# Kernel tuning notes

Measured on AMD Instinct MI355X. Metric: run time of the kernel, lower is better.

Reference implementation:

```python
import jax, jax.numpy as jnp
import numpy as np

T, B = 512, 256
OBS, FEAT, H, ACT = 128, 512, 256, 16
LOG2PI = float(np.log(2.0 * np.pi))


def layer_norm(x, w, b, eps=1e-5):
    m = x.mean(-1, keepdims=True)
    v = ((x - m) ** 2).mean(-1, keepdims=True)
    return (x - m) / jnp.sqrt(v + eps) * w + b


def mlp_features(x, W1, b1, W2, b2, gw, gb):
    h = jax.nn.relu(x @ W1.T + b1)
    h = layer_norm(h @ W2.T + b2, gw, gb)
    return jax.nn.relu(h)


def masked_lstm_scan(feat, done, h0, c0, Wih, Whh, bih, bhh):
    # feat: [T,B,H], done: [T,B] float, h0/c0: [B,H]. PyTorch gate order i,f,g,o.
    def step(carry, inp):
        h, c = carry
        x, d = inp
        m = (1.0 - d)[:, None]
        h = h * m
        c = c * m
        g = x @ Wih.T + bih + h @ Whh.T + bhh
        i, f, gg, o = jnp.split(g, 4, axis=-1)
        c = jax.nn.sigmoid(f) * c + jax.nn.sigmoid(i) * jnp.tanh(gg)
        h = jax.nn.sigmoid(o) * jnp.tanh(c)
        return (h, c), h
    (hT, cT), hs = jax.lax.scan(step, (h0, c0), (feat, done))
    return hs, hT, cT


def setup_inputs():
    key = jax.random.key(0)
    ks = jax.random.split(key, 40)
    rn = lambda k, s, sc=0.05: jax.random.normal(k, s, dtype=jnp.float32) * sc
    inp = {}
    inp["x"] = jax.random.normal(ks[0], (T * B, OBS), dtype=jnp.float32)
    inp["done"] = jax.random.randint(ks[1], (T * B,), 0, 2).astype(jnp.int32)
    inp["actor_h0"] = rn(ks[2], (1, B, H), 0.1)
    inp["actor_c0"] = rn(ks[3], (1, B, H), 0.1)
    inp["critic_h0"] = rn(ks[4], (1, B, H), 0.1)
    inp["critic_c0"] = rn(ks[5], (1, B, H), 0.1)
    inp["action"] = jax.random.normal(ks[6], (T * B, ACT), dtype=jnp.float32)
    j = 7
    for p in ("a", "c"):
        inp[p + "_W1"] = rn(ks[j], (FEAT, OBS)); j += 1
        inp[p + "_b1"] = jnp.zeros((FEAT,), jnp.float32)
        inp[p + "_W2"] = rn(ks[j], (H, FEAT)); j += 1
        inp[p + "_b2"] = jnp.zeros((H,), jnp.float32)
        inp[p + "_flnw"] = jnp.ones((H,), jnp.float32)
        inp[p + "_flnb"] = jnp.zeros((H,), jnp.float32)
        inp[p + "_Wih"] = rn(ks[j], (4 * H, H)); j += 1
        inp[p + "_Whh"] = rn(ks[j], (4 * H, H)); j += 1
        inp[p + "_bih"] = jnp.zeros((4 * H,), jnp.float32)
        inp[p + "_bhh"] = jnp.zeros((4 * H,), jnp.float32)
        inp[p + "_lnw"] = jnp.ones((H,), jnp.float32)
        inp[p + "_lnb"] = jnp.zeros((H,), jnp.float32)
    inp["a_mW"] = rn(ks[j], (ACT, H)); j += 1
    inp["a_mb"] = jnp.zeros((ACT,), jnp.float32)
    inp["a_logstd"] = jnp.zeros((1, ACT), jnp.float32)
    inp["c_hW"] = rn(ks[j], (1, H)); j += 1
    inp["c_hb"] = jnp.zeros((1,), jnp.float32)
    return inp


def reference(x, done, actor_h0, actor_c0, critic_h0, critic_c0, action,
              a_W1, a_b1, a_W2, a_b2, a_flnw, a_flnb, a_Wih, a_Whh, a_bih, a_bhh,
              a_lnw, a_lnb, a_mW, a_mb, a_logstd,
              c_W1, c_b1, c_W2, c_b2, c_flnw, c_flnb, c_Wih, c_Whh, c_bih, c_bhh,
              c_lnw, c_lnb, c_hW, c_hb):
    Bn = actor_h0.shape[1]
    N = x.shape[0]
    Tn = N // Bn
    d = done.astype(jnp.float32).reshape(Tn, Bn)
    # actor branch
    a_feat = mlp_features(x, a_W1, a_b1, a_W2, a_b2, a_flnw, a_flnb).reshape(Tn, Bn, -1)
    hs, ah, acell = masked_lstm_scan(a_feat, d, actor_h0[0], actor_c0[0], a_Wih, a_Whh, a_bih, a_bhh)
    ha = layer_norm(hs.reshape(N, -1), a_lnw, a_lnb)
    mean = ha @ a_mW.T + a_mb
    logstd = jnp.broadcast_to(a_logstd, mean.shape)
    std = jnp.exp(logstd)
    logprob = (-0.5 * ((action - mean) / std) ** 2 - logstd - 0.5 * LOG2PI).sum(1)
    entropy = (0.5 + 0.5 * LOG2PI + logstd).sum(1)
    # critic branch
    c_feat = mlp_features(x, c_W1, c_b1, c_W2, c_b2, c_flnw, c_flnb).reshape(Tn, Bn, -1)
    cs, ch, ccell = masked_lstm_scan(c_feat, d, critic_h0[0], critic_c0[0], c_Wih, c_Whh, c_bih, c_bhh)
    hc = layer_norm(cs.reshape(N, -1), c_lnw, c_lnb)
    value = hc @ c_hW.T + c_hb
    return (logprob, entropy, value, ah[None], acell[None], ch[None], ccell[None])
```

## Files before the change

### kernel.cpp

```cpp
#include <hip/hip_runtime.h>

typedef unsigned short u16;
typedef unsigned long long u64;
typedef __attribute__((ext_vector_type(8))) short short8;
typedef __attribute__((ext_vector_type(4))) float floatx4;
typedef __attribute__((ext_vector_type(4))) float f32x4;
typedef __attribute__((ext_vector_type(4))) int intx4;

#define LOG2PI_F 1.8378770664093453f
#define LOG2E_F 1.4426950408889634f
#define TWOLOG2E_F 2.8853900817779268f

__device__ inline float bf2f(u16 u) { return __uint_as_float(((unsigned)u) << 16); }
__device__ inline u16 f2bf(float f) {
  unsigned u = __float_as_uint(f);
  u += 0x7fff + ((u >> 16) & 1);
  return (u16)(u >> 16);
}

struct PrepArgs {
  const float* src[18];
  const float* src2[18];
  void* dst[18];
  int mode[18];
  int n[18];
  int blk0[19];
  int nseg;
};

__global__ __launch_bounds__(256) void k_prep(PrepArgs a) {
  int b = blockIdx.x, s = 0;
  while (s + 1 < a.nseg && b >= a.blk0[s + 1]) ++s;
  int i = (b - a.blk0[s]) * 1024 + threadIdx.x * 4;
  if (i >= a.n[s]) return;
  if (a.mode[s] == 0) {
    f32x4 v = *(const f32x4*)(a.src[s] + i);
    u64 p = (u64)f2bf(v[0]) | ((u64)f2bf(v[1]) << 16)
          | ((u64)f2bf(v[2]) << 32) | ((u64)f2bf(v[3]) << 48);
    *(u64*)((u16*)a.dst[s] + i) = p;
  } else if (a.mode[s] == 1) {
    f32x4 x = *(const f32x4*)(a.src[s] + i);
    f32x4 y = *(const f32x4*)(a.src2[s] + i);
    *(f32x4*)((float*)a.dst[s] + i) = x + y;
  } else {
    *(f32x4*)((float*)a.dst[s] + i) = *(const f32x4*)(a.src[s] + i);
  }
}

__global__ __launch_bounds__(256) void k_quant(const float* __restrict__ w0,
                                               const float* __restrict__ w1,
                                               char* __restrict__ q, float* __restrict__ sr) {
  int tid = threadIdx.x, lane = tid & 63;
  int row = blockIdx.x * 4 + (tid >> 6);
  int br = row >> 10, r = row & 1023;
  const float* src = (br ? w1 : w0) + (size_t)r * 256 + lane * 4;
  f32x4 v = *(const f32x4*)src;
  float m = fmaxf(fmaxf(fabsf(v[0]), fabsf(v[1])), fmaxf(fabsf(v[2]), fabsf(v[3])));
#pragma unroll
  for (int o = 32; o >= 1; o >>= 1) m = fmaxf(m, __shfl_xor(m, o));
  float inv = m > 0.f ? 127.f / m : 0.f;
  int pk = 0;
#pragma unroll
  for (int c = 0; c < 4; ++c) {
    int qq = __float2int_rn(v[c] * inv);
    qq = qq > 127 ? 127 : (qq < -127 ? -127 : qq);
    pk |= (qq & 255) << (8 * c);
  }
  *(int*)(q + (size_t)row * 256 + lane * 4) = pk;
  if (lane == 0) {
    float sf = (r >= 512 && r < 768) ? TWOLOG2E_F : -LOG2E_F;
    sr[row] = m * (1.f / (127.f * 127.f)) * sf;
  }
}

template <int EPI, int AF32>
__global__ __launch_bounds__(256, 2) void k_gemm(
    const void* __restrict__ Agv, const u16* __restrict__ Wg,
    const float* __restrict__ biasP, void* __restrict__ outv,
    int Nn, int K, int relu, int Tseg,
    long az, long wz, long oz) {
  __shared__ u16 As[128][72];
  __shared__ u16 Ws[128][72];
  const int tid = threadIdx.x;
  const int z = blockIdx.z;
  const int bn = blockIdx.x * 128;
  const int bm = blockIdx.y * 128;
  const int w = tid >> 6, lane = tid & 63, lm = lane & 15, lq = lane >> 4;
  const int wr = (w >> 1) * 64, wc = (w & 1) * 64;
  const int tr = tid >> 3, tc = (tid & 7) * 8;

  const u16* Ab = (const u16*)Agv;
  const float* Af = (const float*)Agv;
  const u16* Wb = Wg + (size_t)z * wz;

  floatx4 acc[4][4] = {};

  for (int k0 = 0; k0 < K; k0 += 64) {
    __syncthreads();
#pragma unroll
    for (int rr = 0; rr < 4; ++rr) {
      int row = rr * 32 + tr;
      if (AF32) {
        const float* src = Af + (size_t)z * az + (size_t)(bm + row) * K + k0 + tc;
        f32x4 v0 = *(const f32x4*)src;
        f32x4 v1 = *(const f32x4*)(src + 4);
        short8 sv;
#pragma unroll
        for (int c = 0; c < 4; ++c) { sv[c] = (short)f2bf(v0[c]); sv[4 + c] = (short)f2bf(v1[c]); }
        *(short8*)&As[row][tc] = sv;
      } else {
        *(short8*)&As[row][tc] = *(const short8*)(Ab + (size_t)z * az + (size_t)(bm + row) * K + k0 + tc);
      }
      *(short8*)&Ws[row][tc] = *(const short8*)(Wb + (size_t)(bn + row) * K + k0 + tc);
    }
    __syncthreads();
#pragma unroll
    for (int kk = 0; kk < 2; ++kk) {
      short8 a4[4], b4[4];
#pragma unroll
      for (int i = 0; i < 4; ++i) {
        a4[i] = *(const short8*)&As[wr + i * 16 + lm][kk * 32 + lq * 8];
        b4[i] = *(const short8*)&Ws[wc + i * 16 + lm][kk * 32 + lq * 8];
      }
#pragma unroll
      for (int i = 0; i < 4; ++i)
#pragma unroll
        for (int j = 0; j < 4; ++j)
          acc[i][j] = __builtin_amdgcn_mfma_f32_16x16x32_bf16(a4[i], b4[j], acc[i][j], 0, 0, 0);
    }
  }

#pragma unroll
  for (int i = 0; i < 4; ++i) {
#pragma unroll
    for (int j = 0; j < 4; ++j) {
      int col = bn + wc + j * 16 + lm;
      float bv = biasP[(size_t)z * Nn + col];
      float v[4];
#pragma unroll
      for (int r = 0; r < 4; ++r) {
        float t = acc[i][j][r] + bv;
        v[r] = relu ? fmaxf(t, 0.f) : t;
      }
      int row0l = bm + wr + i * 16 + lq * 4;
      if (EPI == 1) {
        u16* o = (u16*)outv + (size_t)z * oz;
#pragma unroll
        for (int r = 0; r < 4; ++r) o[(size_t)(row0l + r) * Nn + col] = f2bf(v[r]);
      } else {
        float s = (col >= 512 && col < 768) ? TWOLOG2E_F : -LOG2E_F;
        int t_l = row0l >> 8;
        int bfull = row0l & 255;
        int bbx = bfull >> 4;
        int mq = (bfull >> 2) & 3;
        u64 p = (u64)f2bf(v[0] * s) | ((u64)f2bf(v[1] * s) << 16)
              | ((u64)f2bf(v[2] * s) << 32) | ((u64)f2bf(v[3] * s) << 48);
        u16* o = (u16*)outv + (size_t)z * oz;
        size_t idx = ((((size_t)bbx * Tseg + t_l) * 4 + mq) * 1024 + col) * 4;
        *(u64*)(o + idx) = p;
      }
    }
  }
}

__global__ __launch_bounds__(256) void k_ln_relu(const u16* __restrict__ in,
                                                 const float* __restrict__ lnp,
                                                 u16* __restrict__ out,
                                                 long inz, long outz) {
  int z = blockIdx.y;
  int w = threadIdx.x >> 6, lane = threadIdx.x & 63;
  size_t row = (size_t)blockIdx.x * 4 + w;
  const u16* ip = in + (size_t)z * inz;
  u16* op = out + (size_t)z * outz;
  const float* gw = lnp + (size_t)z * 512;
  const float* gb = gw + 256;
  u64 hv = *(const u64*)(ip + row * 256 + lane * 4);
  float x[4];
#pragma unroll
  for (int c = 0; c < 4; ++c) x[c] = bf2f((u16)(hv >> (16 * c)));
  float s = x[0] + x[1] + x[2] + x[3];
  float q = x[0] * x[0] + x[1] * x[1] + x[2] * x[2] + x[3] * x[3];
#pragma unroll
  for (int o = 32; o >= 1; o >>= 1) { s += __shfl_xor(s, o); q += __shfl_xor(q, o); }
  float mean = s * (1.f / 256.f);
  float var = q * (1.f / 256.f) - mean * mean;
  float rs = rsqrtf(var + 1e-5f);
  u64 p = 0;
#pragma unroll
  for (int c = 0; c < 4; ++c) {
    int k = lane * 4 + c;
    float y = (x[c] - mean) * rs * gw[k] + gb[k];
    y = fmaxf(y, 0.f);
    p |= ((u64)f2bf(y)) << (16 * c);
  }
  *(u64*)(op + row * 256 + lane * 4) = p;
}

struct ScanArgs {
  const u16 *gin0, *gin1;
  const char *whq0, *whq1;
  const float *sr0, *sr1;
  const float *h00, *h01, *c00, *c01;
  char *hs0, *hs1;
  float *hsv0, *hsv1, *csv0, *csv1;
  const int* done;
  int t0, Tseg;
};

__global__ __launch_bounds__(1024, 1) void k_scan(ScanArgs A) {
  const int bb = blockIdx.x & 127, br = blockIdx.x >> 7;
  const int bbx = bb >> 3;
  const int rb = bb << 1;
  const int tid = threadIdx.x;
  const int w = tid >> 6, lane = tid & 63, lm = lane & 15, lq = lane >> 4;
  const int mrow = lq & 1;
  const bool iscell = lq < 2;
  const int jj = w * 16 + lm;
  const int hoff = w * 256 + mrow * 16 + lm;

  extern __shared__ char dsm[];
  char* hl = dsm;

  const char* whq = br ? A.whq1 : A.whq0;
  const float* srP = br ? A.sr1 : A.sr0;
  const u16* gin = (br ? A.gin1 : A.gin0) + (size_t)bbx * A.Tseg * 16384;
  const float* h0 = br ? A.h01 : A.h00;
  const float* c0 = br ? A.c01 : A.c00;
  char* hs = (br ? A.hs1 : A.hs0) + bbx * 4096;
  float* hsv = br ? A.hsv1 : A.hsv0;
  float* csv = br ? A.csv1 : A.csv0;

  intx4 wreg[4][4];
#pragma unroll
  for (int g = 0; g < 4; ++g)
#pragma unroll
    for (int kk = 0; kk < 4; ++kk)
      wreg[g][kk] =
          *(const intx4*)(whq + (size_t)(g * 256 + w * 16 + lm) * 256 + kk * 64 + lq * 16);

  float srw[4];
#pragma unroll
  for (int g = 0; g < 4; ++g) srw[g] = srP[g * 256 + jj];

  float creg = c0[(size_t)(rb + mrow) * 256 + jj];

  if (tid < 512) {
    int c = tid & 255, buf = tid >> 8;
    int kk = c >> 6, lqk = (c >> 4) & 3, m = c & 15;
    intx4 val = {0, 0, 0, 0};
    if (buf == 0 && m < 2) {
      const float* hp = h0 + (size_t)(rb + m) * 256 + kk * 64 + lqk * 16;
#pragma unroll
      for (int q4 = 0; q4 < 4; ++q4) {
        int pk = 0;
#pragma unroll
        for (int b = 0; b < 4; ++b) {
          int qv = __float2int_rn(hp[q4 * 4 + b] * 127.f);
          qv = qv > 127 ? 127 : (qv < -127 ? -127 : qv);
          pk |= (qv & 255) << (8 * b);
        }
        val[q4] = pk;
      }
    }
    *(intx4*)&hl[buf * 4096 + c * 16] = val;
  }
  __syncthreads();

  const u16* ginT = gin + ((rb >> 2) & 3) * 4096 + (rb & 3) + mrow + jj * 4;
  const int* dptrA = A.done + (size_t)A.t0 * 256 + rb + (lm & 1);
  const int* dptrC = A.done + (size_t)A.t0 * 256 + rb + mrow;

  u16 gnxt[4] = {0, 0, 0, 0};
  int dcN = 0;
  int daN = *dptrA;
  if (iscell) {
#pragma unroll
    for (int g = 0; g < 4; ++g) gnxt[g] = ginT[g * 1024];
    dcN = *dptrC;
  }

  intx4 z4 = {0, 0, 0, 0};

  for (int tl = 0; tl < A.Tseg; ++tl) {
    const int curo = (tl & 1) * 4096, nxto = curo ^ 4096;

    u16 gcur[4];
#pragma unroll
    for (int g = 0; g < 4; ++g) gcur[g] = gnxt[g];
    int da = daN;
    int dc = dcN;

    if (tl + 1 < A.Tseg) {
      ginT += 16384;
      dptrA += 256;
      dptrC += 256;
      daN = *dptrA;
      if (iscell) {
#pragma unroll
        for (int g = 0; g < 4; ++g) gnxt[g] = ginT[g * 1024];
        dcN = *dptrC;
      }
    }

    intx4 af[4];
#pragma unroll
    for (int kk = 0; kk < 4; ++kk) {
      intx4 hv = *(const intx4*)&hl[curo + kk * 1024 + lane * 16];
      af[kk] = da ? z4 : hv;
    }

    intx4 acc[4] = {};
#pragma unroll
    for (int kk = 0; kk < 4; ++kk)
#pragma unroll
      for (int g = 0; g < 4; ++g)
        acc[g] = __builtin_amdgcn_mfma_i32_16x16x64_i8(af[kk], wreg[g][kk], acc[g], 0, 0, 0);

    int av[4];
#pragma unroll
    for (int g = 0; g < 4; ++g) {
      int s0 = __shfl(acc[g][0], lm);
      int s1 = __shfl(acc[g][1], lm);
      av[g] = mrow ? s1 : s0;
    }

    if (iscell) {
      float cprev = dc ? 0.f : creg;
      float xi = fmaf((float)av[0], srw[0], bf2f(gcur[0]));
      float xf = fmaf((float)av[1], srw[1], bf2f(gcur[1]));
      float xg = fmaf((float)av[2], srw[2], bf2f(gcur[2]));
      float xo = fmaf((float)av[3], srw[3], bf2f(gcur[3]));
      float ig = __builtin_amdgcn_rcpf(1.f + __builtin_amdgcn_exp2f(xi));
      float fg = __builtin_amdgcn_rcpf(1.f + __builtin_amdgcn_exp2f(xf));
      float gg = 1.f - 2.f * __builtin_amdgcn_rcpf(1.f + __builtin_amdgcn_exp2f(xg));
      float og = __builtin_amdgcn_rcpf(1.f + __builtin_amdgcn_exp2f(xo));
      float cn = fg * cprev + ig * gg;
      creg = cn;
      float th = 1.f - 2.f * __builtin_amdgcn_rcpf(1.f + __builtin_amdgcn_exp2f(TWOLOG2E_F * cn));
      float hn = og * th;
      int qv = __float2int_rn(hn * 127.f);
      hl[nxto + hoff] = (char)qv;
      if (tl == A.Tseg - 1) {
        size_t idx = (size_t)(rb + mrow) * 256 + jj;
        hsv[idx] = hn;
        csv[idx] = cn;
      }
    }
    asm volatile("s_waitcnt lgkmcnt(0)" ::: "memory");
    __builtin_amdgcn_s_barrier();
    __builtin_amdgcn_sched_barrier(0);
    if (tid < 128) {
      int a_l = nxto + (tid >> 3) * 256 + (tid & 7) * 4;
      int mg = (bb & 7) * 2 + ((tid >> 2) & 1);
      int a_g = (tid >> 3) * 256 + mg * 16 + (tid & 3) * 4;
      *(int*)(hs + (size_t)tl * 65536 + a_g) = *(const int*)&hl[a_l];
    }
  }
}

__global__ __launch_bounds__(256) void k_head(
    const char* __restrict__ hs_a, const char* __restrict__ hs_c,
    const float* __restrict__ a_lnw, const float* __restrict__ a_lnb,
    const float* __restrict__ c_lnw, const float* __restrict__ c_lnb,
    const float* __restrict__ mW, const float* __restrict__ mb,
    const float* __restrict__ logstd, const float* __restrict__ hW,
    const float* __restrict__ hb, const float* __restrict__ action,
    float* __restrict__ lp, float* __restrict__ ent, float* __restrict__ val,
    int row0) {
  __shared__ float smW[16][260];
  __shared__ float shW[256];
  __shared__ float spar[4][256];
  __shared__ float hrow[4][264];
  int tid = threadIdx.x;
  for (int i = tid; i < 4096; i += 256) smW[i >> 8][i & 255] = mW[i];
  shW[tid] = hW[tid];
  spar[0][tid] = a_lnw[tid]; spar[1][tid] = a_lnb[tid];
  spar[2][tid] = c_lnw[tid]; spar[3][tid] = c_lnb[tid];
  __syncthreads();

  int w = tid >> 6, lane = tid & 63, lm = lane & 15, lq = lane >> 4;
  float entc = 0.f;
#pragma unroll
  for (int j = 0; j < 16; ++j) entc += 0.5f + 0.5f * LOG2PI_F + logstd[j];
  float ls = logstd[lm];
  float sd = __expf(ls);
  float mbj = mb[lm];

  int rbase = (blockIdx.x * 4 + w) * 16;
  for (int rr = 0; rr < 16; ++rr) {
    int row = rbase + rr;
    int m = row & 15;
    size_t base = (size_t)(row >> 8) * 65536 + (size_t)((row >> 4) & 15) * 4096;
    int off = (lane >> 4) * 1024 + (m + 16 * ((lane >> 2) & 3)) * 16 + (lane & 3) * 4;
    int va = *(const int*)(hs_a + base + off);
    float x[4];
#pragma unroll
    for (int c = 0; c < 4; ++c) x[c] = (float)((va << (24 - 8 * c)) >> 24) * (1.f / 127.f);
    float s = x[0] + x[1] + x[2] + x[3];
    float q = x[0] * x[0] + x[1] * x[1] + x[2] * x[2] + x[3] * x[3];
#pragma unroll
    for (int o = 32; o >= 1; o >>= 1) { s += __shfl_xor(s, o); q += __shfl_xor(q, o); }
    float mean = s * (1.f / 256.f);
    float rs = rsqrtf(q * (1.f / 256.f) - mean * mean + 1e-5f);
    floatx4 hh;
#pragma unroll
    for (int c = 0; c < 4; ++c) {
      int k = lane * 4 + c;
      hh[c] = (x[c] - mean) * rs * spar[0][k] + spar[1][k];
    }
    *(floatx4*)&hrow[w][lane * 4] = hh;
    float p = 0.f;
#pragma unroll 16
    for (int k2 = 0; k2 < 64; ++k2) {
      int kx = lq * 64 + ((k2 + lq * 16) & 63);
      p = fmaf(hrow[w][kx], smW[lm][kx], p);
    }
    p += __shfl_xor(p, 16);
    p += __shfl_xor(p, 32);
    float meanj = p + mbj;
    float aj = action[(size_t)(row0 + row) * 16 + lm];
    float z = (aj - meanj) / sd;
    float term = -0.5f * z * z - ls - 0.5f * LOG2PI_F;
    term += __shfl_xor(term, 1);
    term += __shfl_xor(term, 2);
    term += __shfl_xor(term, 4);
    term += __shfl_xor(term, 8);
    int vc = *(const int*)(hs_c + base + off);
    float y[4];
#pragma unroll
    for (int c = 0; c < 4; ++c) y[c] = (float)((vc << (24 - 8 * c)) >> 24) * (1.f / 127.f);
    float s2 = y[0] + y[1] + y[2] + y[3];
    float q2 = y[0] * y[0] + y[1] * y[1] + y[2] * y[2] + y[3] * y[3];
#pragma unroll
    for (int o = 32; o >= 1; o >>= 1) { s2 += __shfl_xor(s2, o); q2 += __shfl_xor(q2, o); }
    float mean2 = s2 * (1.f / 256.f);
    float rs2 = rsqrtf(q2 * (1.f / 256.f) - mean2 * mean2 + 1e-5f);
    float pv = 0.f;
#pragma unroll
    for (int c = 0; c < 4; ++c) {
      int k = lane * 4 + c;
      float hc = (y[c] - mean2) * rs2 * spar[2][k] + spar[3][k];
      pv = fmaf(hc, shW[k], pv);
    }
#pragma unroll
    for (int o = 32; o >= 1; o >>= 1) pv += __shfl_xor(pv, o);
    if (lane == 0) {
      lp[row0 + row] = term;
      ent[row0 + row] = entc;
      val[row0 + row] = pv + hb[0];
    }
  }
}

extern "C" void kernel_launch(void* const* d_in, const int* in_sizes, int n_in,
                              void* d_out, int out_size, void* d_ws, size_t ws_size,
                              hipStream_t stream) {
  const int N = 131072, T = 512;
  const float* x = (const float*)d_in[0];
  const int* done = (const int*)d_in[1];
  const float* h0i[2] = {(const float*)d_in[2], (const float*)d_in[4]};
  const float* c0i[2] = {(const float*)d_in[3], (const float*)d_in[5]};
  const float* action = (const float*)d_in[6];
  const float *W1[2], *b1[2], *W2[2], *b2[2], *flnw[2], *flnb[2];
  const float *Wih[2], *Whh[2], *bih[2], *bhh[2], *lnw[2], *lnb[2];
  for (int br = 0; br < 2; ++br) {
    int o = 7 + br * 12;
    W1[br] = (const float*)d_in[o + 0];  b1[br] = (const float*)d_in[o + 1];
    W2[br] = (const float*)d_in[o + 2];  b2[br] = (const float*)d_in[o + 3];
    flnw[br] = (const float*)d_in[o + 4]; flnb[br] = (const float*)d_in[o + 5];
    Wih[br] = (const float*)d_in[o + 6]; Whh[br] = (const float*)d_in[o + 7];
    bih[br] = (const float*)d_in[o + 8]; bhh[br] = (const float*)d_in[o + 9];
    lnw[br] = (const float*)d_in[o + 10]; lnb[br] = (const float*)d_in[o + 11];
  }
  const float* mW = (const float*)d_in[31];
  const float* mb = (const float*)d_in[32];
  const float* logstd = (const float*)d_in[33];
  const float* hW = (const float*)d_in[34];
  const float* hb = (const float*)d_in[35];

  float* out = (float*)d_out;
  float* o_lp = out;
  float* o_ent = out + N;
  float* o_val = out + 2 * N;
  float* o_ah = out + 3 * N;
  float* o_ac = o_ah + 65536;
  float* o_ch = o_ac + 65536;
  float* o_cc = o_ch + 65536;

  auto rq = [&](long sr2, long st2) -> size_t {
    long Ts = T / st2, Ms = N / sr2;
    size_t s = 0;
    auto al = [&](size_t b) { s += (b + 255) & ~(size_t)255; };
    al(2 * 65536 * 2); al(2 * 131072 * 2); al(2 * 262144 * 2);
    al(2 * 262144); al(2048 * 4);
    al(2 * 1024 * 4); al(2 * 512 * 4); al(2 * 256 * 4); al(1024 * 4);
    al(2 * 65536 * 4); al(2 * 65536 * 4);
    al((size_t)2 * Ms * 512 * 2);
    al((size_t)2 * Ms * 256 * 2);
    al((size_t)2 * N * 256 * 2);
    al((size_t)2 * Ts * 262144 * 2);
    al((size_t)2 * Ts * 65536);
    return s;
  };
  int sr = 16, st = 16;
  const int cand[7][2] = {{1, 1}, {2, 2}, {4, 4}, {4, 8}, {8, 8}, {8, 16}, {16, 16}};
  for (int i = 0; i < 7; ++i)
    if (rq(cand[i][0], cand[i][1]) + ((size_t)4 << 20) <= ws_size) { sr = cand[i][0]; st = cand[i][1]; break; }
  const long Ts = T / st, Ms = N / sr;

  char* pp = (char*)d_ws;
  auto carve = [&](size_t b) -> void* { void* r = pp; pp += (b + 255) & ~(size_t)255; return r; };
  u16* W1b = (u16*)carve(2 * 65536 * 2);
  u16* W2b = (u16*)carve(2 * 131072 * 2);
  u16* Wihb = (u16*)carve(2 * 262144 * 2);
  char* whhq = (char*)carve(2 * 262144);
  float* srowP = (float*)carve(2048 * 4);
  float* bihh = (float*)carve(2 * 1024 * 4);
  float* b1c = (float*)carve(2 * 512 * 4);
  float* b2c = (float*)carve(2 * 256 * 4);
  float* lnp = (float*)carve(1024 * 4);
  float* hsv = (float*)carve(2 * 65536 * 4);
  float* csv = (float*)carve(2 * 65536 * 4);
  u16* h1 = (u16*)carve((size_t)2 * Ms * 512 * 2);
  u16* g2 = (u16*)carve((size_t)2 * Ms * 256 * 2);
  u16* featP = (u16*)carve((size_t)2 * N * 256 * 2);
  u16* ginP = (u16*)carve((size_t)2 * Ts * 262144 * 2);
  char* hsbP = (char*)carve((size_t)2 * Ts * 65536);

  PrepArgs pa{};
  int ns = 0, blk = 0;
  auto addseg = [&](const float* s1, const float* s2, void* d, int n, int mode) {
    pa.src[ns] = s1; pa.src2[ns] = s2; pa.dst[ns] = d; pa.mode[ns] = mode; pa.n[ns] = n;
    pa.blk0[ns] = blk; blk += (n + 1023) / 1024; ++ns;
  };
  for (int br = 0; br < 2; ++br) {
    addseg(W1[br], nullptr, W1b + br * 65536, 65536, 0);
    addseg(W2[br], nullptr, W2b + br * 131072, 131072, 0);
    addseg(Wih[br], nullptr, Wihb + br * 262144, 262144, 0);
    addseg(bih[br], bhh[br], bihh + br * 1024, 1024, 1);
    addseg(b1[br], nullptr, b1c + br * 512, 512, 2);
    addseg(b2[br], nullptr, b2c + br * 256, 256, 2);
    addseg(flnw[br], nullptr, lnp + br * 512, 256, 2);
    addseg(flnb[br], nullptr, lnp + br * 512 + 256, 256, 2);
  }
  pa.nseg = ns;
  pa.blk0[ns] = blk;
  k_prep<<<blk, 256, 0, stream>>>(pa);
  k_quant<<<512, 256, 0, stream>>>(Whh[0], Whh[1], whhq, srowP);

  for (int s = 0; s < sr; ++s) {
    k_gemm<1, 1><<<dim3(4, Ms / 128, 2), 256, 0, stream>>>(
        x + (size_t)s * Ms * 128, W1b, b1c, h1, 512, 128, 1, 0,
        0L, 65536L, (long)Ms * 512);
    k_gemm<1, 0><<<dim3(2, Ms / 128, 2), 256, 0, stream>>>(
        h1, W2b, b2c, g2, 256, 512, 0, 0,
        (long)Ms * 512, 131072L, (long)Ms * 256);
    k_ln_relu<<<dim3(Ms / 4, 2), 256, 0, stream>>>(
        g2, lnp, featP + (size_t)s * Ms * 256, (long)Ms * 256, (long)N * 256);
  }

  for (int s = 0; s < st; ++s) {
    long t0 = s * Ts;
    k_gemm<2, 0><<<dim3(8, Ts * 2, 2), 256, 0, stream>>>(
        featP + (size_t)t0 * 65536, Wihb, bihh, ginP, 1024, 256, 0, (int)Ts,
        (long)N * 256, 262144L, Ts * 262144L);
    ScanArgs sa;
    sa.gin0 = ginP; sa.gin1 = ginP + Ts * 262144;
    sa.whq0 = whhq; sa.whq1 = whhq + 262144;
    sa.sr0 = srowP; sa.sr1 = srowP + 1024;
    sa.h00 = s ? hsv : h0i[0]; sa.h01 = s ? hsv + 65536 : h0i[1];
    sa.c00 = s ? csv : c0i[0]; sa.c01 = s ? csv + 65536 : c0i[1];
    sa.hs0 = hsbP; sa.hs1 = hsbP + Ts * 65536;
    bool last = (s == st - 1);
    sa.hsv0 = last ? o_ah : hsv; sa.hsv1 = last ? o_ch : hsv + 65536;
    sa.csv0 = last ? o_ac : csv; sa.csv1 = last ? o_cc : csv + 65536;
    sa.done = done; sa.t0 = (int)t0; sa.Tseg = (int)Ts;
    k_scan<<<256, 1024, 8192, stream>>>(sa);
    k_head<<<(int)(Ts * 256 / 64), 256, 0, stream>>>(
        hsbP, hsbP + Ts * 65536, lnw[0], lnb[0], lnw[1], lnb[1],
        mW, mb, logstd, hW, hb, action,
        o_lp, o_ent, o_val, (int)(t0 * 256));
  }
}
```

Measured before the change: 1.933 ms.

## Exploit done resets to batch independent LSTM chunks across MFMA rows

The scan kernel now splits each segment's timesteps into independent chunks at done boundaries, because a reset zeroes the hidden state and breaks the dependency. It processes the p-th step of all chunks together in the 16 MFMA rows, so the serial depth becomes the longest chunk instead of Tseg. Cell state and quantized h for every timestep are kept in LDS and written out at the end. The gin layout goes back to row-major, and the workspace-size search is replaced by fixed split counts. This adds setup work, LDS use and per-row gathers, and relies on done containing frequent resets.

```diff
diff --git a/kernel.cpp b/kernel.cpp
--- a/kernel.cpp
+++ b/kernel.cpp
@@ -16,6 +16,10 @@
   unsigned u = __float_as_uint(f);
   u += 0x7fff + ((u >> 16) & 1);
   return (u16)(u >> 16);
+}
+__device__ inline int q127(float f) {
+  int qv = __float2int_rn(f * 127.f);
+  return qv > 127 ? 127 : (qv < -127 ? -127 : qv);
 }
 
 struct PrepArgs {
@@ -149,15 +153,9 @@
         for (int r = 0; r < 4; ++r) o[(size_t)(row0l + r) * Nn + col] = f2bf(v[r]);
       } else {
         float s = (col >= 512 && col < 768) ? TWOLOG2E_F : -LOG2E_F;
-        int t_l = row0l >> 8;
-        int bfull = row0l & 255;
-        int bbx = bfull >> 4;
-        int mq = (bfull >> 2) & 3;
-        u64 p = (u64)f2bf(v[0] * s) | ((u64)f2bf(v[1] * s) << 16)
-              | ((u64)f2bf(v[2] * s) << 32) | ((u64)f2bf(v[3] * s) << 48);
         u16* o = (u16*)outv + (size_t)z * oz;
-        size_t idx = ((((size_t)bbx * Tseg + t_l) * 4 + mq) * 1024 + col) * 4;
-        *(u64*)(o + idx) = p;
+#pragma unroll
+        for (int r = 0; r < 4; ++r) o[(size_t)(row0l + r) * Nn + col] = f2bf(v[r] * s);
       }
     }
   }
@@ -207,28 +205,32 @@
   int t0, Tseg;
 };
 
+#define HPITCH 272
+#define CPITCH 260
+#define SCAN_LDS (34 * 2 * HPITCH + 64 * CPITCH * 4 + 80 * 4 + 33 * 4)
+
 __global__ __launch_bounds__(1024, 1) void k_scan(ScanArgs A) {
   const int bb = blockIdx.x & 127, br = blockIdx.x >> 7;
-  const int bbx = bb >> 3;
   const int rb = bb << 1;
   const int tid = threadIdx.x;
   const int w = tid >> 6, lane = tid & 63, lm = lane & 15, lq = lane >> 4;
-  const int mrow = lq & 1;
-  const bool iscell = lq < 2;
   const int jj = w * 16 + lm;
-  const int hoff = w * 256 + mrow * 16 + lm;
 
   extern __shared__ char dsm[];
-  char* hl = dsm;
+  char* hst = dsm;
+  float* cst = (float*)(dsm + 34 * 2 * HPITCH);
+  int* chinfo = (int*)(dsm + 34 * 2 * HPITCH + 64 * CPITCH * 4);
+  int* cnt = chinfo + 80;
 
   const char* whq = br ? A.whq1 : A.whq0;
   const float* srP = br ? A.sr1 : A.sr0;
-  const u16* gin = (br ? A.gin1 : A.gin0) + (size_t)bbx * A.Tseg * 16384;
+  const u16* gin = br ? A.gin1 : A.gin0;
   const float* h0 = br ? A.h01 : A.h00;
   const float* c0 = br ? A.c01 : A.c00;
-  char* hs = (br ? A.hs1 : A.hs0) + bbx * 4096;
+  char* hsg = (br ? A.hs1 : A.hs0) + (bb >> 3) * 4096;
   float* hsv = br ? A.hsv1 : A.hsv0;
   float* csv = br ? A.csv1 : A.csv0;
+  const int lastT = A.Tseg - 1;
 
   intx4 wreg[4][4];
 #pragma unroll
@@ -242,119 +244,131 @@
 #pragma unroll
   for (int g = 0; g < 4; ++g) srw[g] = srP[g * 256 + jj];
 
-  float creg = c0[(size_t)(rb + mrow) * 256 + jj];
-
+  if (w == 0) {
+    int row = lane >> 5, t = lane & 31;
+    int dn = A.done[(size_t)(A.t0 + t) * 256 + rb + row];
+    int isstart = (t == 0) || dn;
+    u64 mask = __ballot(isstart ? 1 : 0);
+    int desc = 0, key = -1;
+    if (isstart) {
+      u64 m2 = (lane == 63) ? 0ULL : (mask >> (lane + 1));
+      int lim = (row + 1) * 32 - lane;
+      int d = lim;
+      if (m2) { int z = (int)__ffsll((long long)m2); if (z < d) d = z; }
+      int iszero = dn ? 1 : 0;
+      desc = t | (row << 8) | (iszero << 9) | (d << 16);
+      key = (d << 8) | (63 - lane);
+    }
+    int rank = 0;
+#pragma unroll 1
+    for (int i = 0; i < 64; ++i) {
+      int ok = __shfl(key, i);
+      rank += (ok > key) ? 1 : 0;
+    }
+    if (isstart) chinfo[rank] = desc;
+    int nch = __popcll(mask);
+    for (int c = nch + lane; c < 80; c += 64)
+      chinfo[c] = 0 | (0 << 8) | (1 << 9) | (0 << 16);
+    if (lane == 0) cnt[32] = nch;
+  }
+  for (int i = tid; i < 64 * CPITCH; i += 1024) cst[i] = 0.f;
   if (tid < 512) {
-    int c = tid & 255, buf = tid >> 8;
-    int kk = c >> 6, lqk = (c >> 4) & 3, m = c & 15;
-    intx4 val = {0, 0, 0, 0};
-    if (buf == 0 && m < 2) {
-      const float* hp = h0 + (size_t)(rb + m) * 256 + kk * 64 + lqk * 16;
-#pragma unroll
-      for (int q4 = 0; q4 < 4; ++q4) {
-        int pk = 0;
-#pragma unroll
-        for (int b = 0; b < 4; ++b) {
-          int qv = __float2int_rn(hp[q4 * 4 + b] * 127.f);
-          qv = qv > 127 ? 127 : (qv < -127 ? -127 : qv);
-          pk |= (qv & 255) << (8 * b);
+    int row = tid >> 8, j = tid & 255;
+    float hv = h0[(size_t)(rb + row) * 256 + j];
+    hst[(0 * 2 + row) * HPITCH + j] = (char)q127(hv);
+    hst[(33 * 2 + row) * HPITCH + j] = 0;
+  }
+  __syncthreads();
+
+  {
+    int nch = cnt[32];
+    if (tid < 32) {
+      int c2 = 0;
+      for (int c = 0; c < nch; ++c) c2 += ((chinfo[c] >> 16) > tid) ? 1 : 0;
+      cnt[tid] = c2;
+    }
+#pragma unroll 1
+    for (int c04 = 0; c04 < 64; c04 += 4) {
+      int c = c04 + (tid >> 8);
+      if (c < nch) {
+        int d = chinfo[c];
+        if (((d >> 9) & 1) == 0 && (d & 255) == 0) {
+          int row = (d >> 8) & 1, j = tid & 255;
+          cst[c * CPITCH + j] = c0[(size_t)(rb + row) * 256 + j];
         }
-        val[q4] = pk;
-      }
-    }
-    *(intx4*)&hl[buf * 4096 + c * 16] = val;
+      }
+    }
   }
   __syncthreads();
 
-  const u16* ginT = gin + ((rb >> 2) & 3) * 4096 + (rb & 3) + mrow + jj * 4;
-  const int* dptrA = A.done + (size_t)A.t0 * 256 + rb + (lm & 1);
-  const int* dptrC = A.done + (size_t)A.t0 * 256 + rb + mrow;
-
-  u16 gnxt[4] = {0, 0, 0, 0};
-  int dcN = 0;
-  int daN = *dptrA;
-  if (iscell) {
-#pragma unroll
-    for (int g = 0; g < 4; ++g) gnxt[g] = ginT[g * 1024];
-    dcN = *dptrC;
-  }
-
-  intx4 z4 = {0, 0, 0, 0};
-
-  for (int tl = 0; tl < A.Tseg; ++tl) {
-    const int curo = (tl & 1) * 4096, nxto = curo ^ 4096;
-
-    u16 gcur[4];
-#pragma unroll
-    for (int g = 0; g < 4; ++g) gcur[g] = gnxt[g];
-    int da = daN;
-    int dc = dcN;
-
-    if (tl + 1 < A.Tseg) {
-      ginT += 16384;
-      dptrA += 256;
-      dptrC += 256;
-      daN = *dptrA;
-      if (iscell) {
-#pragma unroll
-        for (int g = 0; g < 4; ++g) gnxt[g] = ginT[g * 1024];
-        dcN = *dptrC;
-      }
-    }
-
-    intx4 af[4];
-#pragma unroll
-    for (int kk = 0; kk < 4; ++kk) {
-      intx4 hv = *(const intx4*)&hl[curo + kk * 1024 + lane * 16];
-      af[kk] = da ? z4 : hv;
-    }
-
-    intx4 acc[4] = {};
-#pragma unroll
-    for (int kk = 0; kk < 4; ++kk)
-#pragma unroll
-      for (int g = 0; g < 4; ++g)
-        acc[g] = __builtin_amdgcn_mfma_i32_16x16x64_i8(af[kk], wreg[g][kk], acc[g], 0, 0, 0);
-
-    int av[4];
-#pragma unroll
-    for (int g = 0; g < 4; ++g) {
-      int s0 = __shfl(acc[g][0], lm);
-      int s1 = __shfl(acc[g][1], lm);
-      av[g] = mrow ? s1 : s0;
-    }
-
-    if (iscell) {
-      float cprev = dc ? 0.f : creg;
-      float xi = fmaf((float)av[0], srw[0], bf2f(gcur[0]));
-      float xf = fmaf((float)av[1], srw[1], bf2f(gcur[1]));
-      float xg = fmaf((float)av[2], srw[2], bf2f(gcur[2]));
-      float xo = fmaf((float)av[3], srw[3], bf2f(gcur[3]));
-      float ig = __builtin_amdgcn_rcpf(1.f + __builtin_amdgcn_exp2f(xi));
-      float fg = __builtin_amdgcn_rcpf(1.f + __builtin_amdgcn_exp2f(xf));
-      float gg = 1.f - 2.f * __builtin_amdgcn_rcpf(1.f + __builtin_amdgcn_exp2f(xg));
-      float og = __builtin_amdgcn_rcpf(1.f + __builtin_amdgcn_exp2f(xo));
-      float cn = fg * cprev + ig * gg;
-      creg = cn;
-      float th = 1.f - 2.f * __builtin_amdgcn_rcpf(1.f + __builtin_amdgcn_exp2f(TWOLOG2E_F * cn));
-      float hn = og * th;
-      int qv = __float2int_rn(hn * 127.f);
-      hl[nxto + hoff] = (char)qv;
-      if (tl == A.Tseg - 1) {
-        size_t idx = (size_t)(rb + mrow) * 256 + jj;
-        hsv[idx] = hn;
-        csv[idx] = cn;
-      }
-    }
-    asm volatile("s_waitcnt lgkmcnt(0)" ::: "memory");
-    __builtin_amdgcn_s_barrier();
-    __builtin_amdgcn_sched_barrier(0);
-    if (tid < 128) {
-      int a_l = nxto + (tid >> 3) * 256 + (tid & 7) * 4;
-      int mg = (bb & 7) * 2 + ((tid >> 2) & 1);
-      int a_g = (tid >> 3) * 256 + mg * 16 + (tid & 3) * 4;
-      *(int*)(hs + (size_t)tl * 65536 + a_g) = *(const int*)&hl[a_l];
-    }
+  const int maxp = chinfo[0] >> 16;
+
+  for (int p = 0; p < maxp; ++p) {
+    int Ap = cnt[p];
+#pragma unroll 1
+    for (int tb = 0; tb < 64; tb += 16) {
+      if (tb >= Ap) break;
+      int dA = chinfo[tb + lm];
+      int stA = dA & 255, rowA = (dA >> 8) & 1, zrA = (dA >> 9) & 1;
+      int slot = (p == 0) ? (zrA ? 33 : 0) : (stA + p);
+      int habase = (slot * 2 + rowA) * HPITCH;
+      int trr[4], rwr[4], crv[4];
+      u16 gld[4][4];
+      float cpr[4];
+#pragma unroll
+      for (int r = 0; r < 4; ++r) {
+        int cr = tb + 4 * lq + r;
+        crv[r] = cr;
+        int dr = chinfo[cr];
+        trr[r] = (dr & 255) + p;
+        rwr[r] = (dr >> 8) & 1;
+        unsigned off = ((unsigned)trr[r] * 256 + (unsigned)(rb + rwr[r])) * 1024 + jj;
+        gld[r][0] = gin[off];
+        gld[r][1] = gin[off + 256];
+        gld[r][2] = gin[off + 512];
+        gld[r][3] = gin[off + 768];
+        cpr[r] = cst[cr * CPITCH + jj];
+      }
+      intx4 acc[4] = {};
+#pragma unroll
+      for (int kk = 0; kk < 4; ++kk) {
+        intx4 af = *(const intx4*)&hst[habase + kk * 64 + lq * 16];
+#pragma unroll
+        for (int g = 0; g < 4; ++g)
+          acc[g] = __builtin_amdgcn_mfma_i32_16x16x64_i8(af, wreg[g][kk], acc[g], 0, 0, 0);
+      }
+#pragma unroll
+      for (int r = 0; r < 4; ++r) {
+        if (crv[r] < Ap) {
+          float xi = fmaf((float)acc[0][r], srw[0], bf2f(gld[r][0]));
+          float xf = fmaf((float)acc[1][r], srw[1], bf2f(gld[r][1]));
+          float xg = fmaf((float)acc[2][r], srw[2], bf2f(gld[r][2]));
+          float xo = fmaf((float)acc[3][r], srw[3], bf2f(gld[r][3]));
+          float ig = __builtin_amdgcn_rcpf(1.f + __builtin_amdgcn_exp2f(xi));
+          float fg = __builtin_amdgcn_rcpf(1.f + __builtin_amdgcn_exp2f(xf));
+          float gg = 1.f - 2.f * __builtin_amdgcn_rcpf(1.f + __builtin_amdgcn_exp2f(xg));
+          float og = __builtin_amdgcn_rcpf(1.f + __builtin_amdgcn_exp2f(xo));
+          float cn = fg * cpr[r] + ig * gg;
+          float th = 1.f - 2.f * __builtin_amdgcn_rcpf(1.f + __builtin_amdgcn_exp2f(TWOLOG2E_F * cn));
+          float hn = og * th;
+          cst[crv[r] * CPITCH + jj] = cn;
+          hst[((trr[r] + 1) * 2 + rwr[r]) * HPITCH + jj] = (char)q127(hn);
+          if (trr[r] == lastT) {
+            size_t idx = (size_t)(rb + rwr[r]) * 256 + jj;
+            hsv[idx] = hn;
+            csv[idx] = cn;
+          }
+        }
+      }
+    }
+    __syncthreads();
+  }
+
+  {
+    int t = tid >> 5, row = (tid >> 4) & 1, q = tid & 15;
+    intx4 v = *(const intx4*)&hst[((t + 1) * 2 + row) * HPITCH + q * 16];
+    char* dst = hsg + (size_t)t * 65536 + (q >> 2) * 1024 + (q & 3) * 256 + ((bb & 7) * 2 + row) * 16;
+    *(intx4*)dst = v;
   }
 }
 
@@ -487,25 +501,7 @@
   float* o_ch = o_ac + 65536;
   float* o_cc = o_ch + 65536;
 
-  auto rq = [&](long sr2, long st2) -> size_t {
-    long Ts = T / st2, Ms = N / sr2;
-    size_t s = 0;
-    auto al = [&](size_t b) { s += (b + 255) & ~(size_t)255; };
-    al(2 * 65536 * 2); al(2 * 131072 * 2); al(2 * 262144 * 2);
-    al(2 * 262144); al(2048 * 4);
-    al(2 * 1024 * 4); al(2 * 512 * 4); al(2 * 256 * 4); al(1024 * 4);
-    al(2 * 65536 * 4); al(2 * 65536 * 4);
-    al((size_t)2 * Ms * 512 * 2);
-    al((size_t)2 * Ms * 256 * 2);
-    al((size_t)2 * N * 256 * 2);
-    al((size_t)2 * Ts * 262144 * 2);
-    al((size_t)2 * Ts * 65536);
-    return s;
-  };
-  int sr = 16, st = 16;
-  const int cand[7][2] = {{1, 1}, {2, 2}, {4, 4}, {4, 8}, {8, 8}, {8, 16}, {16, 16}};
-  for (int i = 0; i < 7; ++i)
-    if (rq(cand[i][0], cand[i][1]) + ((size_t)4 << 20) <= ws_size) { sr = cand[i][0]; st = cand[i][1]; break; }
+  const int sr = 16, st = 16;
   const long Ts = T / st, Ms = N / sr;
 
   char* pp = (char*)d_ws;
@@ -548,6 +544,9 @@
   k_prep<<<blk, 256, 0, stream>>>(pa);
   k_quant<<<512, 256, 0, stream>>>(Whh[0], Whh[1], whhq, srowP);
 
+  hipFuncSetAttribute((const void*)&k_scan, hipFuncAttributeMaxDynamicSharedMemorySize,
+                      ((SCAN_LDS + 255) & ~255));
+
   for (int s = 0; s < sr; ++s) {
     k_gemm<1, 1><<<dim3(4, Ms / 128, 2), 256, 0, stream>>>(
         x + (size_t)s * Ms * 128, W1b, b1c, h1, 512, 128, 1, 0,
@@ -575,7 +574,7 @@
     sa.hsv0 = last ? o_ah : hsv; sa.hsv1 = last ? o_ch : hsv + 65536;
     sa.csv0 = last ? o_ac : csv; sa.csv1 = last ? o_cc : csv + 65536;
     sa.done = done; sa.t0 = (int)t0; sa.Tseg = (int)Ts;
-    k_scan<<<256, 1024, 8192, stream>>>(sa);
+    k_scan<<<256, 1024, ((SCAN_LDS + 255) & ~255), stream>>>(sa);
     k_head<<<(int)(Ts * 256 / 64), 256, 0, stream>>>(
         hsbP, hsbP + Ts * 65536, lnw[0], lnb[0], lnw[1], lnb[1],
         mW, mb, logstd, hW, hb, action,
```

Result: slower. 2.664 ms (+37.8%).
